# Kernel tuning notes

Measured on AMD Instinct MI355X. Metric: run time of the kernel, lower is better.

## Reference

```python
import jax, jax.numpy as jnp
import numpy as np

N = 50000      # nodes
E = 800000     # edges (before self loops)
HID = 128      # hidden_dim
FEAT = 128     # feat_dim
NEG_SLOPE = 0.2
BN_EPS = 1e-5


def setup_inputs() -> dict:
    key = jax.random.key(0)
    ks = jax.random.split(key, 16)
    s = lambda d: 1.0 / np.sqrt(d).astype(np.float32)
    return {
        "x": jax.random.normal(ks[0], (N, HID), jnp.float32),
        "edge_index": jax.random.randint(ks[1], (2, E), 0, N, jnp.int32),
        # GATConv 1 (hidden -> hidden)
        "W1": jax.random.normal(ks[2], (HID, HID), jnp.float32) * s(HID),
        "att_src1": jax.random.normal(ks[3], (HID,), jnp.float32) * s(HID),
        "att_dst1": jax.random.normal(ks[4], (HID,), jnp.float32) * s(HID),
        "b1": jnp.zeros((HID,), jnp.float32),
        # BatchNorm1d(hidden) -- eval mode buffers/params
        "bn_gamma": jnp.ones((HID,), jnp.float32),
        "bn_beta": jnp.zeros((HID,), jnp.float32),
        "bn_mean": jax.random.normal(ks[5], (HID,), jnp.float32) * 0.1,
        "bn_var": jax.random.uniform(ks[6], (HID,), jnp.float32, 0.5, 1.5),
        # GATConv 2 (hidden -> feat)
        "W2": jax.random.normal(ks[7], (HID, FEAT), jnp.float32) * s(HID),
        "att_src2": jax.random.normal(ks[8], (FEAT,), jnp.float32) * s(FEAT),
        "att_dst2": jax.random.normal(ks[9], (FEAT,), jnp.float32) * s(FEAT),
        "b2": jnp.zeros((FEAT,), jnp.float32),
    }


def _gat_conv(x, W, att_src, att_dst, bias, src, dst, n_nodes):
    """PyG GATConv, heads=1: gather -> edge attn -> segment softmax -> scatter."""
    h = x @ W                                   # [N, d_out]
    a_s = h @ att_src                           # [N]
    a_d = h @ att_dst                           # [N]
    e = jax.nn.leaky_relu(a_s[src] + a_d[dst], NEG_SLOPE)  # [E']
    # numerically-stable softmax over incoming edges of each dst node
    e_max = jax.ops.segment_max(e, dst, num_segments=n_nodes)
    ex = jnp.exp(e - e_max[dst])
    denom = jax.ops.segment_sum(ex, dst, num_segments=n_nodes)
    alpha = ex / (denom[dst] + 1e-16)           # [E']
    out = jax.ops.segment_sum(alpha[:, None] * h[src], dst, num_segments=n_nodes)
    return out + bias


def reference(x, edge_index, W1, att_src1, att_dst1, b1,
              bn_gamma, bn_beta, bn_mean, bn_var,
              W2, att_src2, att_dst2, b2):
    n = x.shape[0]
    loops = jnp.arange(n, dtype=edge_index.dtype)
    src = jnp.concatenate([edge_index[0], loops])
    dst = jnp.concatenate([edge_index[1], loops])

    h = jax.nn.relu(_gat_conv(x, W1, att_src1, att_dst1, b1, src, dst, n))
    # BatchNorm1d in eval mode (running stats); dropout is identity in eval
    h = (h - bn_mean) * jax.lax.rsqrt(bn_var + BN_EPS) * bn_gamma + bn_beta
    out = jax.nn.relu(_gat_conv(h, W2, att_src2, att_dst2, b2, src, dst, n))
    return out
```

## Files before the change

### kernel.cpp

```cpp
#include <hip/hip_runtime.h>

typedef unsigned short u16;
typedef unsigned int   u32;

__device__ __forceinline__ float b2f(u16 h){ return __uint_as_float(((u32)h) << 16); }
__device__ __forceinline__ u16   f2b(float f){
  u32 u = __float_as_uint(f);
  u32 r = u + 0x7FFFu + ((u >> 16) & 1u);
  return (u16)(r >> 16);
}
__device__ __forceinline__ float lo16(u32 w){ return b2f((u16)(w & 0xFFFFu)); }
__device__ __forceinline__ float hi16(u32 w){ return b2f((u16)(w >> 16)); }

__global__ void r14_zero(int* p, int n){
  int t = blockIdx.x*blockDim.x + threadIdx.x;
  if (t < n) p[t] = 0;
}

__global__ void r14_hist(const int* ei, int E, int Ep, int* cnt){
  int t = blockIdx.x*blockDim.x + threadIdx.x;
  if (t >= Ep) return;
  int dst = (t < E) ? ei[E + t] : (t - E);
  atomicAdd(&cnt[dst], 1);
}

__global__ void r14_scan1(const int* in, int n, int* incl, int* bsums){
  __shared__ int tmp[256];
  int t = threadIdx.x; int g = blockIdx.x*256 + t;
  int v = (g < n) ? in[g] : 0;
  tmp[t] = v; __syncthreads();
  for (int off = 1; off < 256; off <<= 1){
    int u = (t >= off) ? tmp[t - off] : 0;
    __syncthreads();
    tmp[t] += u;
    __syncthreads();
  }
  if (g < n) incl[g] = tmp[t];
  if (t == 255) bsums[blockIdx.x] = tmp[255];
}

__global__ void r14_scan2(int* bsums, int nb){
  __shared__ int tmp[256];
  int t = threadIdx.x;
  int v = (t < nb) ? bsums[t] : 0;
  tmp[t] = v; __syncthreads();
  for (int off = 1; off < 256; off <<= 1){
    int u = (t >= off) ? tmp[t - off] : 0;
    __syncthreads();
    tmp[t] += u;
    __syncthreads();
  }
  if (t < nb) bsums[t] = tmp[t];
}

__global__ void r14_scan3(const int* incl, const int* cnt, const int* bsums,
                          int n, int Nnodes, int* offs, int* cursor){
  int t = threadIdx.x; int b = blockIdx.x; int g = b*256 + t;
  if (g >= n) return;
  int add = (b > 0) ? bsums[b-1] : 0;
  int ex = incl[g] - cnt[g] + add;
  offs[g] = ex;
  if (g < Nnodes) cursor[g] = ex;
}

__global__ void r14_fill(const int* ei, int E, int Ep, int* cursor, int* csr_src){
  int t = blockIdx.x*blockDim.x + threadIdx.x;
  if (t >= Ep) return;
  int src, dst;
  if (t < E){ src = ei[t]; dst = ei[E + t]; } else { src = t - E; dst = t - E; }
  int pos = atomicAdd(&cursor[dst], 1);
  csr_src[pos] = src;
}

__global__ __launch_bounds__(256)
void r14_gemm(const float* __restrict__ X, const float* __restrict__ W,
              const float* __restrict__ atts, const float* __restrict__ attd,
              u16* __restrict__ HB, float* __restrict__ AS, float* __restrict__ AD,
              int nrows){
  __shared__ float xs[64*128];
  int t = threadIdx.x;
  int r0 = blockIdx.x * 64;
  #pragma unroll
  for (int it = 0; it < 8; ++it){
    int idx = it*256 + t;
    int row = idx >> 5;
    int c4  = (idx & 31) * 4;
    float4 v = {0.f,0.f,0.f,0.f};
    if (r0 + row < nrows) v = *(const float4*)(X + (size_t)(r0+row)*128 + c4);
    *(float4*)&xs[row*128 + c4] = v;
  }
  __syncthreads();

  int cgrp = t & 31, rgrp = t >> 5;
  int col0 = cgrp * 4;
  float acc[8][4];
  #pragma unroll
  for (int r = 0; r < 8; ++r){
    #pragma unroll
    for (int j = 0; j < 4; ++j) acc[r][j] = 0.f;
  }
  #pragma unroll 2
  for (int k = 0; k < 128; k += 4){
    float4 w0 = *(const float4*)(W + (size_t)(k+0)*128 + col0);
    float4 w1 = *(const float4*)(W + (size_t)(k+1)*128 + col0);
    float4 w2 = *(const float4*)(W + (size_t)(k+2)*128 + col0);
    float4 w3 = *(const float4*)(W + (size_t)(k+3)*128 + col0);
    float4 xr[8];
    #pragma unroll
    for (int r = 0; r < 8; ++r) xr[r] = *(const float4*)&xs[(rgrp*8 + r)*128 + k];
    #pragma unroll
    for (int r = 0; r < 8; ++r){
      acc[r][0] = fmaf(xr[r].x, w0.x, acc[r][0]);
      acc[r][1] = fmaf(xr[r].x, w0.y, acc[r][1]);
      acc[r][2] = fmaf(xr[r].x, w0.z, acc[r][2]);
      acc[r][3] = fmaf(xr[r].x, w0.w, acc[r][3]);
      acc[r][0] = fmaf(xr[r].y, w1.x, acc[r][0]);
      acc[r][1] = fmaf(xr[r].y, w1.y, acc[r][1]);
      acc[r][2] = fmaf(xr[r].y, w1.z, acc[r][2]);
      acc[r][3] = fmaf(xr[r].y, w1.w, acc[r][3]);
      acc[r][0] = fmaf(xr[r].z, w2.x, acc[r][0]);
      acc[r][1] = fmaf(xr[r].z, w2.y, acc[r][1]);
      acc[r][2] = fmaf(xr[r].z, w2.z, acc[r][2]);
      acc[r][3] = fmaf(xr[r].z, w2.w, acc[r][3]);
      acc[r][0] = fmaf(xr[r].w, w3.x, acc[r][0]);
      acc[r][1] = fmaf(xr[r].w, w3.y, acc[r][1]);
      acc[r][2] = fmaf(xr[r].w, w3.z, acc[r][2]);
      acc[r][3] = fmaf(xr[r].w, w3.w, acc[r][3]);
    }
  }
  float4 sv = *(const float4*)(atts + col0);
  float4 dv = *(const float4*)(attd + col0);
  #pragma unroll
  for (int r = 0; r < 8; ++r){
    int row = r0 + rgrp*8 + r;
    float ps = acc[r][0]*sv.x + acc[r][1]*sv.y + acc[r][2]*sv.z + acc[r][3]*sv.w;
    float pd = acc[r][0]*dv.x + acc[r][1]*dv.y + acc[r][2]*dv.z + acc[r][3]*dv.w;
    #pragma unroll
    for (int off = 16; off >= 1; off >>= 1){
      ps += __shfl_xor(ps, off);
      pd += __shfl_xor(pd, off);
    }
    if (row < nrows){
      uint2 pb;
      pb.x = (u32)f2b(acc[r][0]) | ((u32)f2b(acc[r][1]) << 16);
      pb.y = (u32)f2b(acc[r][2]) | ((u32)f2b(acc[r][3]) << 16);
      *(uint2*)&HB[(size_t)row*128 + col0] = pb;
      if (cgrp == 0){ AS[row] = ps; AD[row] = pd; }
    }
  }
}

__global__ __launch_bounds__(256)
void r14_aggregate(const u16* __restrict__ HB, const float* __restrict__ AS,
                   const float* __restrict__ AD,
                   const int* __restrict__ offs, const int* __restrict__ csr,
                   const float* __restrict__ bias,
                   const float* __restrict__ gamma_, const float* __restrict__ beta_,
                   const float* __restrict__ mean_, const float* __restrict__ var_,
                   float* __restrict__ outp, int n, int doBN){
  int wid  = (blockIdx.x*256 + threadIdx.x) >> 6;
  int lane = threadIdx.x & 63;
  if (wid >= n) return;
  int beg = offs[wid], end = offs[wid+1];
  int deg = end - beg;
  float ad = AD[wid];
  int c2 = lane*2;
  float a0 = 0.f, a1 = 0.f;

  if (deg <= 64){
    int   my_s = 0;
    float my_e = -3.0e38f;
    int myk = beg + lane;
    bool act = (myk < end);
    if (act){
      my_s = csr[myk];
      float e = AS[my_s] + ad;
      my_e = (e > 0.f) ? e : 0.2f*e;
    }
    float m = my_e;
    #pragma unroll
    for (int off = 32; off >= 1; off >>= 1) m = fmaxf(m, __shfl_xor(m, off));
    float pz = act ? __expf(my_e - m) : 0.f;
    float den = pz;
    #pragma unroll
    for (int off = 32; off >= 1; off >>= 1) den += __shfl_xor(den, off);
    float my_al = pz / (den + 1e-16f);

    int j = 0;
    for (; j + 4 <= deg; j += 4){
      int   s0 = __shfl(my_s, j),   s1 = __shfl(my_s, j+1);
      int   s2 = __shfl(my_s, j+2), s3 = __shfl(my_s, j+3);
      float l0 = __shfl(my_al, j),   l1 = __shfl(my_al, j+1);
      float l2 = __shfl(my_al, j+2), l3 = __shfl(my_al, j+3);
      u32 h0 = *(const u32*)&HB[(size_t)s0*128 + c2];
      u32 h1 = *(const u32*)&HB[(size_t)s1*128 + c2];
      u32 h2 = *(const u32*)&HB[(size_t)s2*128 + c2];
      u32 h3 = *(const u32*)&HB[(size_t)s3*128 + c2];
      a0 = fmaf(l0, lo16(h0), a0); a1 = fmaf(l0, hi16(h0), a1);
      a0 = fmaf(l1, lo16(h1), a0); a1 = fmaf(l1, hi16(h1), a1);
      a0 = fmaf(l2, lo16(h2), a0); a1 = fmaf(l2, hi16(h2), a1);
      a0 = fmaf(l3, lo16(h3), a0); a1 = fmaf(l3, hi16(h3), a1);
    }
    for (; j < deg; ++j){
      int   s = __shfl(my_s, j);
      float l = __shfl(my_al, j);
      u32 hv = *(const u32*)&HB[(size_t)s*128 + c2];
      a0 = fmaf(l, lo16(hv), a0); a1 = fmaf(l, hi16(hv), a1);
    }
  } else {
    float m = -3.0e38f;
    for (int k = beg + lane; k < end; k += 64){
      int s = csr[k];
      float e = AS[s] + ad; e = (e > 0.f) ? e : 0.2f*e;
      m = fmaxf(m, e);
    }
    #pragma unroll
    for (int off = 32; off >= 1; off >>= 1) m = fmaxf(m, __shfl_xor(m, off));
    float den = 0.f;
    for (int k = beg + lane; k < end; k += 64){
      int s = csr[k];
      float e = AS[s] + ad; e = (e > 0.f) ? e : 0.2f*e;
      den += __expf(e - m);
    }
    #pragma unroll
    for (int off = 32; off >= 1; off >>= 1) den += __shfl_xor(den, off);
    float inv = 1.0f / (den + 1e-16f);
    for (int k = beg; k < end; ++k){
      int s = csr[k];
      float e = AS[s] + ad; e = (e > 0.f) ? e : 0.2f*e;
      float al = __expf(e - m) * inv;
      u32 hv = *(const u32*)&HB[(size_t)s*128 + c2];
      a0 = fmaf(al, lo16(hv), a0); a1 = fmaf(al, hi16(hv), a1);
    }
  }

  float v0 = a0 + bias[c2];
  float v1 = a1 + bias[c2+1];
  v0 = fmaxf(v0, 0.f); v1 = fmaxf(v1, 0.f);
  if (doBN){
    float s0 = gamma_[c2]   * rsqrtf(var_[c2]   + 1e-5f);
    float s1 = gamma_[c2+1] * rsqrtf(var_[c2+1] + 1e-5f);
    v0 = (v0 - mean_[c2])*s0   + beta_[c2];
    v1 = (v1 - mean_[c2+1])*s1 + beta_[c2+1];
  }
  float2 o = {v0, v1};
  ((float2*)(outp + (size_t)wid*128))[lane] = o;
}

extern "C" void kernel_launch(void* const* d_in, const int* in_sizes, int n_in,
                              void* d_out, int out_size, void* d_ws, size_t ws_size,
                              hipStream_t stream){
  const float* x   = (const float*)d_in[0];
  const int*   ei  = (const int*)  d_in[1];
  const float* W1  = (const float*)d_in[2];
  const float* as1 = (const float*)d_in[3];
  const float* ad1 = (const float*)d_in[4];
  const float* b1  = (const float*)d_in[5];
  const float* bng = (const float*)d_in[6];
  const float* bnb = (const float*)d_in[7];
  const float* bnm = (const float*)d_in[8];
  const float* bnv = (const float*)d_in[9];
  const float* W2  = (const float*)d_in[10];
  const float* as2 = (const float*)d_in[11];
  const float* ad2 = (const float*)d_in[12];
  const float* b2  = (const float*)d_in[13];
  float* out = (float*)d_out;

  int N  = in_sizes[0] / 128;
  int E  = in_sizes[1] / 2;
  int Ep = E + N;
  if (N <= 0 || E <= 0) return;

  char* base = (char*)d_ws;
  size_t off = 0;
  auto alloc = [&](size_t bytes)->char*{
    off = (off + 255) & ~(size_t)255;
    char* q = base + off; off += bytes; return q;
  };
  float* AS     = (float*)alloc((size_t)N*4);
  float* AD     = (float*)alloc((size_t)N*4);
  int*   cnt    = (int*)  alloc((size_t)(N+1)*4);
  int*   offs   = (int*)  alloc((size_t)(N+1)*4);
  int*   cursor = (int*)  alloc((size_t)N*4);
  int*   bsums  = (int*)  alloc(1024);
  int*   csr    = (int*)  alloc((size_t)Ep*4);
  u16*   hb     = (u16*)  alloc((size_t)N*128*2);
  float* x2     = (float*)alloc((size_t)N*128*4);

  int n1 = N + 1;
  int zb = (n1 + 255)/256;
  int eb = (Ep + 255)/256;
  int sb = (n1 + 255)/256;

  r14_zero <<<zb, 256, 0, stream>>>(cnt, n1);
  r14_hist <<<eb, 256, 0, stream>>>(ei, E, Ep, cnt);
  r14_scan1<<<sb, 256, 0, stream>>>(cnt, n1, offs, bsums);
  r14_scan2<<<1, 256, 0, stream>>>(bsums, sb);
  r14_scan3<<<sb, 256, 0, stream>>>(offs, cnt, bsums, n1, N, offs, cursor);
  r14_fill <<<eb, 256, 0, stream>>>(ei, E, Ep, cursor, csr);

  int gb = (N + 63)/64;
  int wb = (N + 3)/4;

  r14_gemm     <<<gb, 256, 0, stream>>>(x, W1, as1, ad1, hb, AS, AD, N);
  r14_aggregate<<<wb, 256, 0, stream>>>(hb, AS, AD, offs, csr, b1, bng, bnb, bnm, bnv,
                                        x2, N, 1);
  r14_gemm     <<<gb, 256, 0, stream>>>(x2, W2, as2, ad2, hb, AS, AD, N);
  r14_aggregate<<<wb, 256, 0, stream>>>(hb, AS, AD, offs, csr, b2, 0, 0, 0, 0,
                                        out, N, 0);
}
```

Measured before the change: 333.7 us.

## Fuse CSR fill into first GEMM launch, shrink GEMM tile, unroll gather by 8

```diff
diff --git a/kernel.cpp b/kernel.cpp
--- a/kernel.cpp
+++ b/kernel.cpp
@@ -12,19 +12,19 @@
 __device__ __forceinline__ float lo16(u32 w){ return b2f((u16)(w & 0xFFFFu)); }
 __device__ __forceinline__ float hi16(u32 w){ return b2f((u16)(w >> 16)); }
 
-__global__ void r14_zero(int* p, int n){
+__global__ void r16_zero(int* p, int n){
   int t = blockIdx.x*blockDim.x + threadIdx.x;
   if (t < n) p[t] = 0;
 }
 
-__global__ void r14_hist(const int* ei, int E, int Ep, int* cnt){
+__global__ void r16_hist(const int* ei, int E, int Ep, int* cnt){
   int t = blockIdx.x*blockDim.x + threadIdx.x;
   if (t >= Ep) return;
   int dst = (t < E) ? ei[E + t] : (t - E);
   atomicAdd(&cnt[dst], 1);
 }
 
-__global__ void r14_scan1(const int* in, int n, int* incl, int* bsums){
+__global__ void r16_scan1(const int* in, int n, int* incl, int* bsums){
   __shared__ int tmp[256];
   int t = threadIdx.x; int g = blockIdx.x*256 + t;
   int v = (g < n) ? in[g] : 0;
@@ -39,7 +39,7 @@
   if (t == 255) bsums[blockIdx.x] = tmp[255];
 }
 
-__global__ void r14_scan2(int* bsums, int nb){
+__global__ void r16_scan2(int* bsums, int nb){
   __shared__ int tmp[256];
   int t = threadIdx.x;
   int v = (t < nb) ? bsums[t] : 0;
@@ -53,7 +53,7 @@
   if (t < nb) bsums[t] = tmp[t];
 }
 
-__global__ void r14_scan3(const int* incl, const int* cnt, const int* bsums,
+__global__ void r16_scan3(const int* incl, const int* cnt, const int* bsums,
                           int n, int Nnodes, int* offs, int* cursor){
   int t = threadIdx.x; int b = blockIdx.x; int g = b*256 + t;
   if (g >= n) return;
@@ -63,25 +63,15 @@
   if (g < Nnodes) cursor[g] = ex;
 }
 
-__global__ void r14_fill(const int* ei, int E, int Ep, int* cursor, int* csr_src){
-  int t = blockIdx.x*blockDim.x + threadIdx.x;
-  if (t >= Ep) return;
-  int src, dst;
-  if (t < E){ src = ei[t]; dst = ei[E + t]; } else { src = t - E; dst = t - E; }
-  int pos = atomicAdd(&cursor[dst], 1);
-  csr_src[pos] = src;
-}
-
-__global__ __launch_bounds__(256)
-void r14_gemm(const float* __restrict__ X, const float* __restrict__ W,
-              const float* __restrict__ atts, const float* __restrict__ attd,
-              u16* __restrict__ HB, float* __restrict__ AS, float* __restrict__ AD,
-              int nrows){
-  __shared__ float xs[64*128];
+__device__ __forceinline__ void r16_gemm_body(
+    const float* __restrict__ X, const float* __restrict__ W,
+    const float* __restrict__ atts, const float* __restrict__ attd,
+    u16* __restrict__ HB, float* __restrict__ AS, float* __restrict__ AD,
+    int nrows, int blk, float* xs){
   int t = threadIdx.x;
-  int r0 = blockIdx.x * 64;
+  int r0 = blk * 32;
   #pragma unroll
-  for (int it = 0; it < 8; ++it){
+  for (int it = 0; it < 4; ++it){
     int idx = it*256 + t;
     int row = idx >> 5;
     int c4  = (idx & 31) * 4;
@@ -93,9 +83,9 @@
 
   int cgrp = t & 31, rgrp = t >> 5;
   int col0 = cgrp * 4;
-  float acc[8][4];
+  float acc[4][4];
   #pragma unroll
-  for (int r = 0; r < 8; ++r){
+  for (int r = 0; r < 4; ++r){
     #pragma unroll
     for (int j = 0; j < 4; ++j) acc[r][j] = 0.f;
   }
@@ -105,11 +95,11 @@
     float4 w1 = *(const float4*)(W + (size_t)(k+1)*128 + col0);
     float4 w2 = *(const float4*)(W + (size_t)(k+2)*128 + col0);
     float4 w3 = *(const float4*)(W + (size_t)(k+3)*128 + col0);
-    float4 xr[8];
-    #pragma unroll
-    for (int r = 0; r < 8; ++r) xr[r] = *(const float4*)&xs[(rgrp*8 + r)*128 + k];
-    #pragma unroll
-    for (int r = 0; r < 8; ++r){
+    float4 xr[4];
+    #pragma unroll
+    for (int r = 0; r < 4; ++r) xr[r] = *(const float4*)&xs[(rgrp*4 + r)*128 + k];
+    #pragma unroll
+    for (int r = 0; r < 4; ++r){
       acc[r][0] = fmaf(xr[r].x, w0.x, acc[r][0]);
       acc[r][1] = fmaf(xr[r].x, w0.y, acc[r][1]);
       acc[r][2] = fmaf(xr[r].x, w0.z, acc[r][2]);
@@ -131,8 +121,8 @@
   float4 sv = *(const float4*)(atts + col0);
   float4 dv = *(const float4*)(attd + col0);
   #pragma unroll
-  for (int r = 0; r < 8; ++r){
-    int row = r0 + rgrp*8 + r;
+  for (int r = 0; r < 4; ++r){
+    int row = r0 + rgrp*4 + r;
     float ps = acc[r][0]*sv.x + acc[r][1]*sv.y + acc[r][2]*sv.z + acc[r][3]*sv.w;
     float pd = acc[r][0]*dv.x + acc[r][1]*dv.y + acc[r][2]*dv.z + acc[r][3]*dv.w;
     #pragma unroll
@@ -151,7 +141,37 @@
 }
 
 __global__ __launch_bounds__(256)
-void r14_aggregate(const u16* __restrict__ HB, const float* __restrict__ AS,
+void r16_gemm_fill(const float* __restrict__ X, const float* __restrict__ W,
+                   const float* __restrict__ atts, const float* __restrict__ attd,
+                   u16* __restrict__ HB, float* __restrict__ AS, float* __restrict__ AD,
+                   int nrows, int gemmBlocks,
+                   const int* __restrict__ ei, int E, int Ep,
+                   int* cursor, int* csr_src){
+  __shared__ float xs[32*128];
+  if ((int)blockIdx.x >= gemmBlocks){
+    int g = ((int)blockIdx.x - gemmBlocks)*256 + threadIdx.x;
+    if (g < Ep){
+      int src, dst;
+      if (g < E){ src = ei[g]; dst = ei[E + g]; } else { src = g - E; dst = g - E; }
+      int pos = atomicAdd(&cursor[dst], 1);
+      csr_src[pos] = src;
+    }
+    return;
+  }
+  r16_gemm_body(X, W, atts, attd, HB, AS, AD, nrows, blockIdx.x, xs);
+}
+
+__global__ __launch_bounds__(256)
+void r16_gemm(const float* __restrict__ X, const float* __restrict__ W,
+              const float* __restrict__ atts, const float* __restrict__ attd,
+              u16* __restrict__ HB, float* __restrict__ AS, float* __restrict__ AD,
+              int nrows){
+  __shared__ float xs[32*128];
+  r16_gemm_body(X, W, atts, attd, HB, AS, AD, nrows, blockIdx.x, xs);
+}
+
+__global__ __launch_bounds__(256)
+void r16_aggregate(const u16* __restrict__ HB, const float* __restrict__ AS,
                    const float* __restrict__ AD,
                    const int* __restrict__ offs, const int* __restrict__ csr,
                    const float* __restrict__ bias,
@@ -187,6 +207,32 @@
     float my_al = pz / (den + 1e-16f);
 
     int j = 0;
+    for (; j + 8 <= deg; j += 8){
+      int   s0 = __shfl(my_s, j),   s1 = __shfl(my_s, j+1);
+      int   s2 = __shfl(my_s, j+2), s3 = __shfl(my_s, j+3);
+      int   s4 = __shfl(my_s, j+4), s5 = __shfl(my_s, j+5);
+      int   s6 = __shfl(my_s, j+6), s7 = __shfl(my_s, j+7);
+      float l0 = __shfl(my_al, j),   l1 = __shfl(my_al, j+1);
+      float l2 = __shfl(my_al, j+2), l3 = __shfl(my_al, j+3);
+      float l4 = __shfl(my_al, j+4), l5 = __shfl(my_al, j+5);
+      float l6 = __shfl(my_al, j+6), l7 = __shfl(my_al, j+7);
+      u32 h0 = *(const u32*)&HB[(size_t)s0*128 + c2];
+      u32 h1 = *(const u32*)&HB[(size_t)s1*128 + c2];
+      u32 h2 = *(const u32*)&HB[(size_t)s2*128 + c2];
+      u32 h3 = *(const u32*)&HB[(size_t)s3*128 + c2];
+      u32 h4 = *(const u32*)&HB[(size_t)s4*128 + c2];
+      u32 h5 = *(const u32*)&HB[(size_t)s5*128 + c2];
+      u32 h6 = *(const u32*)&HB[(size_t)s6*128 + c2];
+      u32 h7 = *(const u32*)&HB[(size_t)s7*128 + c2];
+      a0 = fmaf(l0, lo16(h0), a0); a1 = fmaf(l0, hi16(h0), a1);
+      a0 = fmaf(l1, lo16(h1), a0); a1 = fmaf(l1, hi16(h1), a1);
+      a0 = fmaf(l2, lo16(h2), a0); a1 = fmaf(l2, hi16(h2), a1);
+      a0 = fmaf(l3, lo16(h3), a0); a1 = fmaf(l3, hi16(h3), a1);
+      a0 = fmaf(l4, lo16(h4), a0); a1 = fmaf(l4, hi16(h4), a1);
+      a0 = fmaf(l5, lo16(h5), a0); a1 = fmaf(l5, hi16(h5), a1);
+      a0 = fmaf(l6, lo16(h6), a0); a1 = fmaf(l6, hi16(h6), a1);
+      a0 = fmaf(l7, lo16(h7), a0); a1 = fmaf(l7, hi16(h7), a1);
+    }
     for (; j + 4 <= deg; j += 4){
       int   s0 = __shfl(my_s, j),   s1 = __shfl(my_s, j+1);
       int   s2 = __shfl(my_s, j+2), s3 = __shfl(my_s, j+3);
@@ -291,21 +337,20 @@
   int zb = (n1 + 255)/256;
   int eb = (Ep + 255)/256;
   int sb = (n1 + 255)/256;
-
-  r14_zero <<<zb, 256, 0, stream>>>(cnt, n1);
-  r14_hist <<<eb, 256, 0, stream>>>(ei, E, Ep, cnt);
-  r14_scan1<<<sb, 256, 0, stream>>>(cnt, n1, offs, bsums);
-  r14_scan2<<<1, 256, 0, stream>>>(bsums, sb);
-  r14_scan3<<<sb, 256, 0, stream>>>(offs, cnt, bsums, n1, N, offs, cursor);
-  r14_fill <<<eb, 256, 0, stream>>>(ei, E, Ep, cursor, csr);
-
-  int gb = (N + 63)/64;
+  int gb = (N + 31)/32;
   int wb = (N + 3)/4;
 
-  r14_gemm     <<<gb, 256, 0, stream>>>(x, W1, as1, ad1, hb, AS, AD, N);
-  r14_aggregate<<<wb, 256, 0, stream>>>(hb, AS, AD, offs, csr, b1, bng, bnb, bnm, bnv,
+  r16_zero <<<zb, 256, 0, stream>>>(cnt, n1);
+  r16_hist <<<eb, 256, 0, stream>>>(ei, E, Ep, cnt);
+  r16_scan1<<<sb, 256, 0, stream>>>(cnt, n1, offs, bsums);
+  r16_scan2<<<1, 256, 0, stream>>>(bsums, sb);
+  r16_scan3<<<sb, 256, 0, stream>>>(offs, cnt, bsums, n1, N, offs, cursor);
+
+  r16_gemm_fill<<<gb + eb, 256, 0, stream>>>(x, W1, as1, ad1, hb, AS, AD, N, gb,
+                                             ei, E, Ep, cursor, csr);
+  r16_aggregate<<<wb, 256, 0, stream>>>(hb, AS, AD, offs, csr, b1, bng, bnb, bnm, bnv,
                                         x2, N, 1);
-  r14_gemm     <<<gb, 256, 0, stream>>>(x2, W2, as2, ad2, hb, AS, AD, N);
-  r14_aggregate<<<wb, 256, 0, stream>>>(hb, AS, AD, offs, csr, b2, 0, 0, 0, 0,
+  r16_gemm     <<<gb, 256, 0, stream>>>(x2, W2, as2, ad2, hb, AS, AD, N);
+  r16_aggregate<<<wb, 256, 0, stream>>>(hb, AS, AD, offs, csr, b2, 0, 0, 0, 0,
                                         out, N, 0);
 }
```

New measurement: 313.1 us. 1.07x faster.
